# Kernel optimization log

Measured on AMD Instinct MI355X. Metric: run time of the kernel, lower is better.

## Reference

```python
import jax, jax.numpy as jnp
import numpy as np

NUM_EMBED = 1024
NUM_HEADS = 16
NUM_LAYER = 8
BLOCK_SIZE = 1024
VOCAB = 32000
B, T = 4, 1024
HEAD_SIZE = NUM_EMBED // NUM_HEADS


def _ln(x, g, b, eps=1e-5):
    mu = jnp.mean(x, axis=-1, keepdims=True)
    var = jnp.var(x, axis=-1, keepdims=True)
    return (x - mu) * jax.lax.rsqrt(var + eps) * g + b


def setup_inputs() -> dict:
    key = jax.random.key(0)
    ks = jax.random.split(key, 16)
    C, L, V = NUM_EMBED, NUM_LAYER, VOCAB
    std = 0.02
    n = lambda k, shp: jax.random.normal(k, shp, jnp.float32) * std
    return {
        "x": jax.random.randint(ks[0], (B, T), 0, V),
        "tok_emb": n(ks[1], (V, C)),
        "pos_emb": n(ks[2], (BLOCK_SIZE, C)),
        "Wq": n(ks[3], (L, C, C)),
        "Wk": n(ks[4], (L, C, C)),
        "Wv": n(ks[5], (L, C, C)),
        "Wproj": n(ks[6], (L, C, C)),
        "bproj": jnp.zeros((L, C), jnp.float32),
        "ln1_g": jnp.ones((L, C), jnp.float32),
        "ln1_b": jnp.zeros((L, C), jnp.float32),
        "ln2_g": jnp.ones((L, C), jnp.float32),
        "ln2_b": jnp.zeros((L, C), jnp.float32),
        "W1": n(ks[7], (L, C, 4 * C)),
        "b1": jnp.zeros((L, 4 * C), jnp.float32),
        "W2": n(ks[8], (L, 4 * C, C)),
        "b2": jnp.zeros((L, C), jnp.float32),
        "lnf_g": jnp.ones((C,), jnp.float32),
        "lnf_b": jnp.zeros((C,), jnp.float32),
        "Whead": n(ks[9], (C, V)),
    }


def _forward(x, tok_emb, pos_emb, Wq, Wk, Wv, Wproj, bproj,
             ln1_g, ln1_b, ln2_g, ln2_b, W1, b1, W2, b2,
             lnf_g, lnf_b, Whead):
    Bc, Tc = x.shape
    H, hs = NUM_HEADS, HEAD_SIZE
    h = tok_emb[x] + pos_emb[:Tc]  # [B,T,C]
    causal = jnp.tril(jnp.ones((Tc, Tc), bool))
    neg_inf = jnp.finfo(h.dtype).min
    for l in range(NUM_LAYER):
        xn = _ln(h, ln1_g[l], ln1_b[l])
        q = (xn @ Wq[l]).reshape(Bc, Tc, H, hs)
        k = (xn @ Wk[l]).reshape(Bc, Tc, H, hs)
        v = (xn @ Wv[l]).reshape(Bc, Tc, H, hs)
        att = jnp.einsum('bqhd,bkhd->bhqk', q, k) * (hs ** -0.5)
        att = jnp.where(causal, att, neg_inf)
        att = jax.nn.softmax(att, axis=-1)  # dropout p=0 in eval
        o = jnp.einsum('bhqk,bkhd->bqhd', att, v).reshape(Bc, Tc, H * hs)
        h = h + o @ Wproj[l] + bproj[l]
        xn = _ln(h, ln2_g[l], ln2_b[l])
        h = h + jax.nn.relu(xn @ W1[l] + b1[l]) @ W2[l] + b2[l]
    h = _ln(h, lnf_g, lnf_b)
    return h @ Whead  # logits [B,T,V]


def reference(x, tok_emb, pos_emb, Wq, Wk, Wv, Wproj, bproj,
              ln1_g, ln1_b, ln2_g, ln2_b, W1, b1, W2, b2,
              lnf_g, lnf_b, Whead):
    return _forward(x, tok_emb, pos_emb, Wq, Wk, Wv, Wproj, bproj,
                    ln1_g, ln1_b, ln2_g, ln2_b, W1, b1, W2, b2,
                    lnf_g, lnf_b, Whead)
```

## Files before the change

### kernel.cpp

```cpp
#include <hip/hip_runtime.h>
#include <stdint.h>
#include <stddef.h>

#define C_DIM 1024
#define T_DIM 1024
#define B_DIM 4
#define L_DIM 8
#define V_DIM 32000
#define HS 64
#define NHEAD 16
#define NROWS (B_DIM * T_DIM)
#define LDQ   3072
#define PROWS 65536

typedef __bf16 bf16_t;
typedef __attribute__((ext_vector_type(8))) __bf16 bf16x8;
typedef __attribute__((ext_vector_type(4))) __bf16 bf16x4;
typedef __attribute__((ext_vector_type(4))) float f32x4;
typedef unsigned int u32;
typedef unsigned short u16;

static __device__ __forceinline__ f32x4 mfma16(bf16x8 a, bf16x8 b, f32x4 c) {
    return __builtin_amdgcn_mfma_f32_16x16x32_bf16(a, b, c, 0, 0, 0);
}

static __device__ __forceinline__ void gl_lds16(const bf16_t* g, bf16_t* l) {
    __builtin_amdgcn_global_load_lds(
        (const __attribute__((address_space(1))) u32*)(const void*)g,
        (__attribute__((address_space(3))) u32*)(void*)l, 16, 0, 0);
}

__global__ __launch_bounds__(256) void embed_kernel(
    const int* __restrict__ x, const float* __restrict__ tok,
    const float* __restrict__ pos, float* __restrict__ h) {
    int idx = blockIdx.x * 256 + threadIdx.x;
    int row = idx >> 8;
    int c4  = (idx & 255) * 4;
    int t   = row & (T_DIM - 1);
    int tk  = x[row];
    float4 a = *(const float4*)(tok + (size_t)tk * C_DIM + c4);
    float4 p = *(const float4*)(pos + (size_t)t * C_DIM + c4);
    float4 r;
    r.x = a.x + p.x; r.y = a.y + p.y; r.z = a.z + p.z; r.w = a.w + p.w;
    *(float4*)(h + (size_t)row * C_DIM + c4) = r;
}

static __device__ __forceinline__ void wtr_tile(
    const float* __restrict__ in, bf16_t* __restrict__ out,
    int K, int N, int n0, int k0, int tid) {
    __shared__ float t[64][65];
    int tx = tid & 63, tw = tid >> 6;
#pragma unroll 4
    for (int i = 0; i < 16; ++i) {
        int k = tw * 16 + i;
        t[k][tx] = in[(size_t)(k0 + k) * N + n0 + tx];
    }
    __syncthreads();
#pragma unroll 4
    for (int i = 0; i < 16; ++i) {
        int n = tw * 16 + i;
        out[(size_t)(n0 + n) * K + k0 + tx] = (bf16_t)t[tx][n];
    }
}

__global__ __launch_bounds__(256) void wtr_kernel(
    const float* __restrict__ in, bf16_t* __restrict__ out, int K, int N) {
    wtr_tile(in, out, K, N, blockIdx.x * 64, blockIdx.y * 64, threadIdx.x);
}

__global__ __launch_bounds__(256) void ln_wtr_kernel(
    const float* __restrict__ x, const float* __restrict__ gam,
    const float* __restrict__ bet, bf16_t* __restrict__ out,
    const float* __restrict__ Wq, const float* __restrict__ Wk,
    const float* __restrict__ Wv, const float* __restrict__ Wp,
    const float* __restrict__ W1, const float* __restrict__ W2,
    bf16_t* __restrict__ qkvT, bf16_t* __restrict__ projT,
    bf16_t* __restrict__ w1T, bf16_t* __restrict__ w2T) {
    int bid = blockIdx.x;
    if (bid >= 1024) {
        int b = bid - 1024;
        const float* in; bf16_t* o2; int K, N, tn, tk;
        if (b < 1024) {
            int which = b >> 8, t = b & 255;
            in = which == 0 ? Wq : which == 1 ? Wk : which == 2 ? Wv : Wp;
            o2 = which < 3 ? qkvT + (size_t)which * C_DIM * C_DIM : projT;
            K = C_DIM; N = C_DIM; tn = t & 15; tk = t >> 4;
        } else if (b < 2048) {
            int t = b - 1024; in = W1; o2 = w1T;
            K = C_DIM; N = 4 * C_DIM; tn = t & 63; tk = t >> 6;
        } else {
            int t = b - 2048; in = W2; o2 = w2T;
            K = 4 * C_DIM; N = C_DIM; tn = t & 15; tk = t >> 4;
        }
        wtr_tile(in, o2, K, N, tn * 64, tk * 64, threadIdx.x);
        return;
    }
    int wave = threadIdx.x >> 6, lane = threadIdx.x & 63;
    int row  = bid * 4 + wave;
    const float* xr = x + (size_t)row * C_DIM;
    float4 v[4];
    float s = 0.f, sq = 0.f;
#pragma unroll
    for (int i = 0; i < 4; ++i) {
        v[i] = *(const float4*)(xr + i * 256 + lane * 4);
        s  += v[i].x + v[i].y + v[i].z + v[i].w;
        sq += v[i].x * v[i].x + v[i].y * v[i].y + v[i].z * v[i].z + v[i].w * v[i].w;
    }
#pragma unroll
    for (int m = 1; m < 64; m <<= 1) {
        s  += __shfl_xor(s, m);
        sq += __shfl_xor(sq, m);
    }
    float mu  = s * (1.f / 1024.f);
    float var = sq * (1.f / 1024.f) - mu * mu;
    float rs  = rsqrtf(var + 1e-5f);
    bf16_t* orow = out + (size_t)row * C_DIM;
#pragma unroll
    for (int i = 0; i < 4; ++i) {
        int c = i * 256 + lane * 4;
        float4 g4 = *(const float4*)(gam + c);
        float4 b4 = *(const float4*)(bet + c);
        bf16x4 o;
        o[0] = (bf16_t)((v[i].x - mu) * rs * g4.x + b4.x);
        o[1] = (bf16_t)((v[i].y - mu) * rs * g4.y + b4.y);
        o[2] = (bf16_t)((v[i].z - mu) * rs * g4.z + b4.z);
        o[3] = (bf16_t)((v[i].w - mu) * rs * g4.w + b4.w);
        *(bf16x4*)(orow + c) = o;
    }
}

__global__ __launch_bounds__(256) void ln_kernel(
    const float* __restrict__ x, const float* __restrict__ gam,
    const float* __restrict__ bet, bf16_t* __restrict__ out) {
    int wave = threadIdx.x >> 6, lane = threadIdx.x & 63;
    int row  = blockIdx.x * 4 + wave;
    const float* xr = x + (size_t)row * C_DIM;
    float4 v[4];
    float s = 0.f, sq = 0.f;
#pragma unroll
    for (int i = 0; i < 4; ++i) {
        v[i] = *(const float4*)(xr + i * 256 + lane * 4);
        s  += v[i].x + v[i].y + v[i].z + v[i].w;
        sq += v[i].x * v[i].x + v[i].y * v[i].y + v[i].z * v[i].z + v[i].w * v[i].w;
    }
#pragma unroll
    for (int m = 1; m < 64; m <<= 1) {
        s  += __shfl_xor(s, m);
        sq += __shfl_xor(sq, m);
    }
    float mu  = s * (1.f / 1024.f);
    float var = sq * (1.f / 1024.f) - mu * mu;
    float rs  = rsqrtf(var + 1e-5f);
    bf16_t* orow = out + (size_t)row * C_DIM;
#pragma unroll
    for (int i = 0; i < 4; ++i) {
        int c = i * 256 + lane * 4;
        float4 g4 = *(const float4*)(gam + c);
        float4 b4 = *(const float4*)(bet + c);
        bf16x4 o;
        o[0] = (bf16_t)((v[i].x - mu) * rs * g4.x + b4.x);
        o[1] = (bf16_t)((v[i].y - mu) * rs * g4.y + b4.y);
        o[2] = (bf16_t)((v[i].z - mu) * rs * g4.z + b4.z);
        o[3] = (bf16_t)((v[i].w - mu) * rs * g4.w + b4.w);
        *(bf16x4*)(orow + c) = o;
    }
}

template <int MODE>
__global__ __launch_bounds__(256) void gemm_kernel(
    const bf16_t* __restrict__ A, const bf16_t* __restrict__ Bt,
    const float* __restrict__ bias, void* __restrict__ Cout,
    int M, int N, int K, int KS) {
    __shared__ bf16_t Asm[2][128 * 32];
    __shared__ bf16_t Bsm[2][128 * 32];

    const int tid  = threadIdx.x;
    const int nwg  = gridDim.x;
    int bid = blockIdx.x;
    if ((nwg & 7) == 0) {
        int cpx = nwg >> 3;
        bid = (bid & 7) * cpx + (bid >> 3);
    }
    const int MT = M >> 7;
    const int nblk = MT * (N >> 7);
    const int kp = bid / nblk;
    bid %= nblk;
    const int mt = bid % MT, nt = bid / MT;
    const int mbase = mt << 7, nbase = nt << 7;
    const int wave = tid >> 6, lane = tid & 63;
    const int lr = lane & 15, lg = lane >> 4;
    const int wm = wave >> 1, wn = wave & 1;
    const int KL = K / KS;
    const int koff = kp * KL;
    const int NK = KL >> 5;

    const int srow = lane >> 2;
    const int ssw  = (((lane & 3) ^ ((lane >> 3) & 3)) << 3);
    const bf16_t* aRow = A  + (size_t)(mbase + wave * 32 + srow) * K + koff + ssw;
    const bf16_t* bRow = Bt + (size_t)(nbase + wave * 32 + srow) * K + koff + ssw;
    const int ldsW = wave * 1024;

#define STAGE(buf, kt)                                                        \
    do {                                                                      \
        const bf16_t* ag = aRow + (size_t)(kt) * 32;                          \
        const bf16_t* bg = bRow + (size_t)(kt) * 32;                          \
        gl_lds16(ag,            &Asm[buf][ldsW]);                             \
        gl_lds16(ag + 16 * K,   &Asm[buf][ldsW + 512]);                       \
        gl_lds16(bg,            &Bsm[buf][ldsW]);                             \
        gl_lds16(bg + 16 * K,   &Bsm[buf][ldsW + 512]);                       \
    } while (0)

    STAGE(0, 0);
    __syncthreads();

    f32x4 acc[4][4] = {};
    const int rsw = ((lg ^ ((lr >> 1) & 3)) << 3);
    int buf = 0;
    for (int kt = 0; kt < NK; ++kt) {
        if (kt + 1 < NK) STAGE(buf ^ 1, kt + 1);
        bf16x8 af[4], bfr[4];
#pragma unroll
        for (int i = 0; i < 4; ++i)
            af[i] = *(const bf16x8*)&Asm[buf][(wm * 64 + i * 16 + lr) * 32 + rsw];
#pragma unroll
        for (int j = 0; j < 4; ++j)
            bfr[j] = *(const bf16x8*)&Bsm[buf][(wn * 64 + j * 16 + lr) * 32 + rsw];
#pragma unroll
        for (int i = 0; i < 4; ++i)
#pragma unroll
            for (int j = 0; j < 4; ++j)
                acc[i][j] = mfma16(af[i], bfr[j], acc[i][j]);
        __syncthreads();
        buf ^= 1;
    }
#undef STAGE

    float bj[4];
#pragma unroll
    for (int j = 0; j < 4; ++j)
        bj[j] = (bias && kp == 0) ? bias[nbase + wn * 64 + j * 16 + lr] : 0.0f;
#pragma unroll
    for (int i = 0; i < 4; ++i) {
#pragma unroll
        for (int j = 0; j < 4; ++j) {
            int col = nbase + wn * 64 + j * 16 + lr;
#pragma unroll
            for (int e = 0; e < 4; ++e) {
                int row = mbase + wm * 64 + i * 16 + lg * 4 + e;
                float val = acc[i][j][e] + bj[j];
                size_t off = (size_t)row * N + col;
                if (MODE == 0) {
                    ((bf16_t*)Cout)[off] = (bf16_t)val;
                } else if (MODE == 1) {
                    ((bf16_t*)Cout)[off] = (bf16_t)fmaxf(val, 0.0f);
                } else {
                    atomicAdd(&((float*)Cout)[off], val);
                }
            }
        }
    }
}

template <int MODE>
__global__ __launch_bounds__(512, 4) void gemmW_kernel(
    const bf16_t* __restrict__ A, const bf16_t* __restrict__ Bt,
    const float* __restrict__ bias, void* __restrict__ Cout,
    int M, int N, int K) {
    __shared__ __align__(16) char smem[49152];
    bf16_t (*As)[128 * 32] = (bf16_t(*)[128 * 32])smem;
    bf16_t (*Bs)[256 * 32] = (bf16_t(*)[256 * 32])(smem + 16384);

    const int tid  = threadIdx.x;
    const int nwg  = gridDim.x;
    int bid = blockIdx.x;
    if ((nwg & 7) == 0) {
        int cpx = nwg >> 3;
        bid = (bid & 7) * cpx + (bid >> 3);
    }
    const int MT = M >> 7;
    const int mt = bid % MT, nt = bid / MT;
    const int mbase = mt << 7, nbase = nt << 8;
    const int wave = tid >> 6, lane = tid & 63;
    const int lr = lane & 15, lg = lane >> 4;
    const int wm64 = (wave >> 2) * 64;
    const int wn64 = (wave & 3) * 64;
    const int NK = K >> 5;

    const int srow = tid >> 2;
    const int csrc = (((tid & 3) ^ ((tid >> 3) & 3)) << 3);
    const bf16_t* aPtr = A  + (size_t)(mbase + srow) * K + csrc;
    const bf16_t* b0   = Bt + (size_t)(nbase + srow) * K + csrc;
    const bf16_t* b1   = b0 + (size_t)128 * K;
    const int ldsW = wave * 512;

#define STAGEW(buf, kt)                                                       \
    do {                                                                      \
        gl_lds16(aPtr + (size_t)(kt) * 32, &As[buf][ldsW]);                   \
        gl_lds16(b0   + (size_t)(kt) * 32, &Bs[buf][ldsW]);                   \
        gl_lds16(b1   + (size_t)(kt) * 32, &Bs[buf][4096 + ldsW]);            \
    } while (0)

    STAGEW(0, 0);
    __syncthreads();

    f32x4 acc[4][4] = {};
    const int rofs = ((lg ^ ((lr >> 1) & 3)) << 3);
    int buf = 0;
    for (int kt = 0; kt < NK; ++kt) {
        if (kt + 1 < NK) STAGEW(buf ^ 1, kt + 1);
        bf16x8 af[4], bfr[4];
#pragma unroll
        for (int i = 0; i < 4; ++i)
            af[i] = *(const bf16x8*)&As[buf][(wm64 + i * 16 + lr) * 32 + rofs];
#pragma unroll
        for (int j = 0; j < 4; ++j)
            bfr[j] = *(const bf16x8*)&Bs[buf][(wn64 + j * 16 + lr) * 32 + rofs];
#pragma unroll
        for (int i = 0; i < 4; ++i)
#pragma unroll
            for (int j = 0; j < 4; ++j)
                acc[i][j] = mfma16(af[i], bfr[j], acc[i][j]);
        __syncthreads();
        buf ^= 1;
    }
#undef STAGEW

    float bj[4];
#pragma unroll
    for (int j = 0; j < 4; ++j)
        bj[j] = bias ? bias[nbase + wn64 + j * 16 + lr] : 0.0f;

    if (MODE == 3) {
        float* tw = (float*)smem + wave * (16 * 68);
#pragma unroll
        for (int i = 0; i < 4; ++i) {
#pragma unroll
            for (int j = 0; j < 4; ++j)
#pragma unroll
                for (int e = 0; e < 4; ++e)
                    tw[(lg * 4 + e) * 68 + j * 16 + lr] = acc[i][j][e] + bj[j];
            asm volatile("s_waitcnt lgkmcnt(0)" ::: "memory");
#pragma unroll
            for (int ss = 0; ss < 4; ++ss) {
                int rr = ss * 4 + lg;
                f32x4 v = *(const f32x4*)&tw[rr * 68 + lr * 4];
                size_t off = (size_t)(mbase + wm64 + i * 16 + rr) * N
                           + (nbase + wn64 + lr * 4);
                __builtin_nontemporal_store(v, (f32x4*)&((float*)Cout)[off]);
            }
            asm volatile("s_waitcnt lgkmcnt(0)" ::: "memory");
        }
        return;
    }

#pragma unroll
    for (int i = 0; i < 4; ++i) {
#pragma unroll
        for (int j = 0; j < 4; ++j) {
            int col = nbase + wn64 + j * 16 + lr;
#pragma unroll
            for (int e = 0; e < 4; ++e) {
                int row = mbase + wm64 + i * 16 + lg * 4 + e;
                float val = acc[i][j][e] + bj[j];
                size_t off = (size_t)row * N + col;
                if (MODE == 0) {
                    ((bf16_t*)Cout)[off] = (bf16_t)val;
                } else {
                    ((bf16_t*)Cout)[off] = (bf16_t)fmaxf(val, 0.0f);
                }
            }
        }
    }
}

__global__ __launch_bounds__(256) void attn_kernel(
    const bf16_t* __restrict__ Qb, const bf16_t* __restrict__ Kb,
    const bf16_t* __restrict__ Vb, float* __restrict__ Opart,
    float* __restrict__ Lbuf) {
    __shared__ bf16_t Ksm[2][64][72];
    __shared__ bf16_t Vsm[2][64][72];
    __shared__ bf16_t Psm[4][32][72];

    const int tid  = threadIdx.x;
    const int bid  = blockIdx.x;
    const int rank = bid >> 6;
    const int qt   = 7 - (rank >> 1);
    const int half = rank & 1;
    const int bh   = bid & 63;
    const int hh   = bh & 15;
    const int bb   = bh >> 4;
    const int t0   = half ? (qt + 1) : 0;
    const int t1   = half ? (2 * qt + 2) : (qt + 1);
    const int wave = tid >> 6, lane = tid & 63;
    const int lr = lane & 15, lg = lane >> 4;
    const int qbase = qt * 128 + wave * 32;
    const size_t basei = ((size_t)bb * T_DIM) * LDQ + hh * HS;
    const int pg = bh * 8 + qt;

    bf16x8 qf[2][2];
#pragma unroll
    for (int rb = 0; rb < 2; ++rb) {
        const bf16_t* qrow = Qb + basei + (size_t)(qbase + rb * 16 + lr) * LDQ;
        qf[rb][0] = *(const bf16x8*)(qrow + lg * 8);
        qf[rb][1] = *(const bf16x8*)(qrow + 32 + lg * 8);
    }

    f32x4 o[2][4] = {};
    float psum[2][4];
#pragma unroll
    for (int rb = 0; rb < 2; ++rb)
#pragma unroll
        for (int e = 0; e < 4; ++e) psum[rb][e] = 0.f;

    const int krow = tid >> 2, kc = (tid & 3) * 8;
    const bf16_t* kgp = Kb + basei + (size_t)krow * LDQ + kc;
    const int vds = (tid & 7) * 8, vkg = (tid >> 3) * 2;
    const bf16_t* vgp0 = Vb + basei + (size_t)vkg * LDQ + vds;
    const bf16_t* vgp1 = vgp0 + LDQ;

    uint4 k0r, k1r, v0r, v1r;
    {
        const size_t g0 = (size_t)t0 * 64 * LDQ;
        k0r = *(const uint4*)(kgp + g0);
        k1r = *(const uint4*)(kgp + g0 + 32);
        v0r = *(const uint4*)(vgp0 + g0);
        v1r = *(const uint4*)(vgp1 + g0);
    }
    *(uint4*)&Ksm[0][krow][kc]      = k0r;
    *(uint4*)&Ksm[0][krow][kc + 32] = k1r;
    {
        const u16* e0 = (const u16*)&v0r;
        const u16* e1 = (const u16*)&v1r;
#pragma unroll
        for (int j = 0; j < 8; ++j)
            *(u32*)&Vsm[0][vds + j][vkg] = (u32)e0[j] | ((u32)e1[j] << 16);
    }
    __syncthreads();

    const float SCL = 0.18033688011112042f;
    for (int kt = t0; kt < t1; ++kt) {
        const int c = (kt - t0) & 1;
        if (kt + 1 < t1) {
            const size_t go = (size_t)(kt + 1) * 64 * LDQ;
            k0r = *(const uint4*)(kgp + go);
            k1r = *(const uint4*)(kgp + go + 32);
            v0r = *(const uint4*)(vgp0 + go);
            v1r = *(const uint4*)(vgp1 + go);
        }

        f32x4 s[2][4];
        __builtin_amdgcn_s_setprio(1);
#pragma unroll
        for (int kk = 0; kk < 4; ++kk) {
            bf16x8 kf0 = *(const bf16x8*)&Ksm[c][kk * 16 + lr][lg * 8];
            bf16x8 kf1 = *(const bf16x8*)&Ksm[c][kk * 16 + lr][32 + lg * 8];
#pragma unroll
            for (int rb = 0; rb < 2; ++rb) {
                f32x4 z = {};
                z = mfma16(qf[rb][0], kf0, z);
                z = mfma16(qf[rb][1], kf1, z);
                s[rb][kk] = z;
            }
        }
        __builtin_amdgcn_s_setprio(0);
        if (kt * 64 + 63 > qbase) {
#pragma unroll
            for (int rb = 0; rb < 2; ++rb)
#pragma unroll
                for (int kk = 0; kk < 4; ++kk)
#pragma unroll
                    for (int e = 0; e < 4; ++e) {
                        int key = kt * 64 + kk * 16 + lr;
                        int qi  = qbase + rb * 16 + lg * 4 + e;
                        float v = s[rb][kk][e] * SCL;
                        s[rb][kk][e] = (key <= qi) ? v : -1e30f;
                    }
        } else {
#pragma unroll
            for (int rb = 0; rb < 2; ++rb)
#pragma unroll
                for (int kk = 0; kk < 4; ++kk)
#pragma unroll
                    for (int e = 0; e < 4; ++e)
                        s[rb][kk][e] *= SCL;
        }

#pragma unroll
        for (int rb = 0; rb < 2; ++rb) {
#pragma unroll
            for (int e = 0; e < 4; ++e) {
                float p0 = exp2f(s[rb][0][e]);
                float p1 = exp2f(s[rb][1][e]);
                float p2 = exp2f(s[rb][2][e]);
                float p3 = exp2f(s[rb][3][e]);
                int qrow = rb * 16 + lg * 4 + e;
                Psm[wave][qrow][lr]      = (bf16_t)p0;
                Psm[wave][qrow][16 + lr] = (bf16_t)p1;
                Psm[wave][qrow][32 + lr] = (bf16_t)p2;
                Psm[wave][qrow][48 + lr] = (bf16_t)p3;
                psum[rb][e] += (p0 + p1) + (p2 + p3);
            }
        }

        asm volatile("s_waitcnt lgkmcnt(0)" ::: "memory");
        bf16x8 pf[2][2];
#pragma unroll
        for (int rb = 0; rb < 2; ++rb)
#pragma unroll
            for (int h2 = 0; h2 < 2; ++h2)
                pf[rb][h2] = *(const bf16x8*)&Psm[wave][rb * 16 + lr][h2 * 32 + lg * 8];
        __builtin_amdgcn_s_setprio(1);
#pragma unroll
        for (int h2 = 0; h2 < 2; ++h2)
#pragma unroll
            for (int db = 0; db < 4; ++db) {
                bf16x8 vf = *(const bf16x8*)&Vsm[c][db * 16 + lr][h2 * 32 + lg * 8];
#pragma unroll
                for (int rb = 0; rb < 2; ++rb)
                    o[rb][db] = mfma16(pf[rb][h2], vf, o[rb][db]);
            }
        __builtin_amdgcn_s_setprio(0);

        if (kt + 1 < t1) {
            const int w = c ^ 1;
            *(uint4*)&Ksm[w][krow][kc]      = k0r;
            *(uint4*)&Ksm[w][krow][kc + 32] = k1r;
            const u16* e0 = (const u16*)&v0r;
            const u16* e1 = (const u16*)&v1r;
#pragma unroll
            for (int j = 0; j < 8; ++j)
                *(u32*)&Vsm[w][vds + j][vkg] = (u32)e0[j] | ((u32)e1[j] << 16);
        }
        __syncthreads();
    }

    const size_t prow0 = (size_t)half * PROWS + (size_t)pg * 128 + wave * 32;
#pragma unroll
    for (int rb = 0; rb < 2; ++rb)
#pragma unroll
        for (int e = 0; e < 4; ++e) {
            float l = psum[rb][e];
            l += __shfl_xor(l, 1);
            l += __shfl_xor(l, 2);
            l += __shfl_xor(l, 4);
            l += __shfl_xor(l, 8);
            size_t row = prow0 + rb * 16 + lg * 4 + e;
            float* op = Opart + row * 64;
#pragma unroll
            for (int db = 0; db < 4; ++db)
                op[db * 16 + lr] = o[rb][db][e];
            if (lr == 0) Lbuf[row] = l;
        }
}

__global__ __launch_bounds__(256) void attn_merge_kernel(
    const float* __restrict__ Opart, const float* __restrict__ Lbuf,
    bf16_t* __restrict__ Ob) {
    int idx = blockIdx.x * 256 + threadIdx.x;
    int row = idx >> 4, d4 = (idx & 15) * 4;
    float l0 = Lbuf[row];
    float l1 = Lbuf[(size_t)PROWS + row];
    float inv = 1.0f / (l0 + l1);
    float4 a = *(const float4*)&Opart[(size_t)row * 64 + d4];
    float4 b = *(const float4*)&Opart[((size_t)PROWS + row) * 64 + d4];
    bf16x4 r;
    r[0] = (bf16_t)((a.x + b.x) * inv);
    r[1] = (bf16_t)((a.y + b.y) * inv);
    r[2] = (bf16_t)((a.z + b.z) * inv);
    r[3] = (bf16_t)((a.w + b.w) * inv);
    int pg = row >> 7, rloc = row & 127;
    int bh = pg >> 3, qt = pg & 7;
    int bb = bh >> 4, hh = bh & 15;
    *(bf16x4*)&Ob[((size_t)bb * T_DIM + qt * 128 + rloc) * C_DIM + hh * HS + d4] = r;
}

extern "C" void kernel_launch(void* const* d_in, const int* in_sizes, int n_in,
                              void* d_out, int out_size, void* d_ws, size_t ws_size,
                              hipStream_t stream) {
    const int*   x      = (const int*)d_in[0];
    const float* tok    = (const float*)d_in[1];
    const float* pos    = (const float*)d_in[2];
    const float* Wq     = (const float*)d_in[3];
    const float* Wk     = (const float*)d_in[4];
    const float* Wv     = (const float*)d_in[5];
    const float* Wproj  = (const float*)d_in[6];
    const float* bproj  = (const float*)d_in[7];
    const float* ln1_g  = (const float*)d_in[8];
    const float* ln1_b  = (const float*)d_in[9];
    const float* ln2_g  = (const float*)d_in[10];
    const float* ln2_b  = (const float*)d_in[11];
    const float* W1     = (const float*)d_in[12];
    const float* b1     = (const float*)d_in[13];
    const float* W2     = (const float*)d_in[14];
    const float* b2     = (const float*)d_in[15];
    const float* lnf_g  = (const float*)d_in[16];
    const float* lnf_b  = (const float*)d_in[17];
    const float* Whead  = (const float*)d_in[18];
    float* out = (float*)d_out;

    char* ws = (char*)d_ws;
    float*  h    = (float*)ws;   ws += (size_t)NROWS * C_DIM * 4;
    bf16_t* xn   = (bf16_t*)ws;  ws += (size_t)NROWS * C_DIM * 2;
    bf16_t* qkvb = (bf16_t*)ws;  ws += (size_t)NROWS * LDQ * 2;
    bf16_t* ob   = (bf16_t*)ws;  ws += (size_t)NROWS * C_DIM * 2;
    bf16_t* mid  = (bf16_t*)ws;  ws += (size_t)NROWS * 4 * C_DIM * 2;
    bf16_t* wT   = (bf16_t*)ws;  ws += (size_t)V_DIM * C_DIM * 2;
    float*  opart = (float*)ws;  ws += (size_t)2 * PROWS * 64 * 4;
    float*  lbuf  = (float*)ws;  ws += (size_t)2 * PROWS * 4;

    const size_t M1 = (size_t)C_DIM * C_DIM;
    bf16_t* qkvT  = wT;
    bf16_t* projT = wT + 3 * M1;
    bf16_t* w1T   = wT + 4 * M1;
    bf16_t* w2T   = wT + 8 * M1;

    dim3 blk(256);
    dim3 blk512(512);

    embed_kernel<<<dim3(NROWS * C_DIM / 1024), blk, 0, stream>>>(x, tok, pos, h);

    for (int l = 0; l < L_DIM; ++l) {
        const size_t wo  = (size_t)l * M1;
        const size_t wo1 = (size_t)l * 4 * M1;

        ln_wtr_kernel<<<dim3(1024 + 3072), blk, 0, stream>>>(
            h, ln1_g + l * C_DIM, ln1_b + l * C_DIM, xn,
            Wq + wo, Wk + wo, Wv + wo, Wproj + wo, W1 + wo1, W2 + wo1,
            qkvT, projT, w1T, w2T);

        gemmW_kernel<0><<<dim3(32 * 12), blk512, 0, stream>>>(
            xn, qkvT, nullptr, qkvb, NROWS, LDQ, C_DIM);

        attn_kernel<<<dim3(1024), blk, 0, stream>>>(
            qkvb, qkvb + C_DIM, qkvb + 2 * C_DIM, opart, lbuf);
        attn_merge_kernel<<<dim3(PROWS * 16 / 256), blk, 0, stream>>>(
            opart, lbuf, ob);

        gemm_kernel<2><<<dim3(32 * 8 * 2), blk, 0, stream>>>(
            ob, projT, bproj + l * C_DIM, h, NROWS, C_DIM, C_DIM, 2);

        ln_kernel<<<dim3(NROWS / 4), blk, 0, stream>>>(h, ln2_g + l * C_DIM, ln2_b + l * C_DIM, xn);

        gemmW_kernel<1><<<dim3(32 * 16), blk512, 0, stream>>>(
            xn, w1T, b1 + (size_t)l * 4 * C_DIM, mid, NROWS, 4 * C_DIM, C_DIM);

        gemm_kernel<2><<<dim3(32 * 8 * 2), blk, 0, stream>>>(
            mid, w2T, b2 + l * C_DIM, h, NROWS, C_DIM, 4 * C_DIM, 2);
    }

    ln_kernel<<<dim3(NROWS / 4), blk, 0, stream>>>(h, lnf_g, lnf_b, xn);
    wtr_kernel<<<dim3(500, 16), blk, 0, stream>>>(Whead, wT, C_DIM, V_DIM);
    gemmW_kernel<3><<<dim3(32 * 125), blk512, 0, stream>>>(
        xn, wT, nullptr, out, NROWS, V_DIM, C_DIM);
}
```

Before: 2.301 ms.

## Drop split-K attention and merge kernel; each block handles full key range

```diff
diff --git a/kernel.cpp b/kernel.cpp
--- a/kernel.cpp
+++ b/kernel.cpp
@@ -11,7 +11,6 @@
 #define NHEAD 16
 #define NROWS (B_DIM * T_DIM)
 #define LDQ   3072
-#define PROWS 65536
 
 typedef __bf16 bf16_t;
 typedef __attribute__((ext_vector_type(8))) __bf16 bf16x8;
@@ -375,27 +374,23 @@
 
 __global__ __launch_bounds__(256) void attn_kernel(
     const bf16_t* __restrict__ Qb, const bf16_t* __restrict__ Kb,
-    const bf16_t* __restrict__ Vb, float* __restrict__ Opart,
-    float* __restrict__ Lbuf) {
+    const bf16_t* __restrict__ Vb, bf16_t* __restrict__ Ob) {
     __shared__ bf16_t Ksm[2][64][72];
     __shared__ bf16_t Vsm[2][64][72];
     __shared__ bf16_t Psm[4][32][72];
 
     const int tid  = threadIdx.x;
     const int bid  = blockIdx.x;
-    const int rank = bid >> 6;
-    const int qt   = 7 - (rank >> 1);
-    const int half = rank & 1;
+    const int qt   = 7 - (bid >> 6);
     const int bh   = bid & 63;
     const int hh   = bh & 15;
     const int bb   = bh >> 4;
-    const int t0   = half ? (qt + 1) : 0;
-    const int t1   = half ? (2 * qt + 2) : (qt + 1);
+    const int nkt  = 2 * qt + 2;
     const int wave = tid >> 6, lane = tid & 63;
     const int lr = lane & 15, lg = lane >> 4;
     const int qbase = qt * 128 + wave * 32;
     const size_t basei = ((size_t)bb * T_DIM) * LDQ + hh * HS;
-    const int pg = bh * 8 + qt;
+    const size_t baseo = ((size_t)bb * T_DIM) * C_DIM + hh * HS;
 
     bf16x8 qf[2][2];
 #pragma unroll
@@ -419,13 +414,10 @@
     const bf16_t* vgp1 = vgp0 + LDQ;
 
     uint4 k0r, k1r, v0r, v1r;
-    {
-        const size_t g0 = (size_t)t0 * 64 * LDQ;
-        k0r = *(const uint4*)(kgp + g0);
-        k1r = *(const uint4*)(kgp + g0 + 32);
-        v0r = *(const uint4*)(vgp0 + g0);
-        v1r = *(const uint4*)(vgp1 + g0);
-    }
+    k0r = *(const uint4*)(kgp);
+    k1r = *(const uint4*)(kgp + 32);
+    v0r = *(const uint4*)(vgp0);
+    v1r = *(const uint4*)(vgp1);
     *(uint4*)&Ksm[0][krow][kc]      = k0r;
     *(uint4*)&Ksm[0][krow][kc + 32] = k1r;
     {
@@ -438,9 +430,9 @@
     __syncthreads();
 
     const float SCL = 0.18033688011112042f;
-    for (int kt = t0; kt < t1; ++kt) {
-        const int c = (kt - t0) & 1;
-        if (kt + 1 < t1) {
+    for (int kt = 0; kt < nkt; ++kt) {
+        const int c = kt & 1;
+        if (kt + 1 < nkt) {
             const size_t go = (size_t)(kt + 1) * 64 * LDQ;
             k0r = *(const uint4*)(kgp + go);
             k1r = *(const uint4*)(kgp + go + 32);
@@ -521,7 +513,7 @@
             }
         __builtin_amdgcn_s_setprio(0);
 
-        if (kt + 1 < t1) {
+        if (kt + 1 < nkt) {
             const int w = c ^ 1;
             *(uint4*)&Ksm[w][krow][kc]      = k0r;
             *(uint4*)&Ksm[w][krow][kc + 32] = k1r;
@@ -534,7 +526,6 @@
         __syncthreads();
     }
 
-    const size_t prow0 = (size_t)half * PROWS + (size_t)pg * 128 + wave * 32;
 #pragma unroll
     for (int rb = 0; rb < 2; ++rb)
 #pragma unroll
@@ -544,34 +535,12 @@
             l += __shfl_xor(l, 2);
             l += __shfl_xor(l, 4);
             l += __shfl_xor(l, 8);
-            size_t row = prow0 + rb * 16 + lg * 4 + e;
-            float* op = Opart + row * 64;
+            float inv = 1.0f / l;
+            bf16_t* orow = Ob + baseo + (size_t)(qbase + rb * 16 + lg * 4 + e) * C_DIM;
 #pragma unroll
             for (int db = 0; db < 4; ++db)
-                op[db * 16 + lr] = o[rb][db][e];
-            if (lr == 0) Lbuf[row] = l;
-        }
-}
-
-__global__ __launch_bounds__(256) void attn_merge_kernel(
-    const float* __restrict__ Opart, const float* __restrict__ Lbuf,
-    bf16_t* __restrict__ Ob) {
-    int idx = blockIdx.x * 256 + threadIdx.x;
-    int row = idx >> 4, d4 = (idx & 15) * 4;
-    float l0 = Lbuf[row];
-    float l1 = Lbuf[(size_t)PROWS + row];
-    float inv = 1.0f / (l0 + l1);
-    float4 a = *(const float4*)&Opart[(size_t)row * 64 + d4];
-    float4 b = *(const float4*)&Opart[((size_t)PROWS + row) * 64 + d4];
-    bf16x4 r;
-    r[0] = (bf16_t)((a.x + b.x) * inv);
-    r[1] = (bf16_t)((a.y + b.y) * inv);
-    r[2] = (bf16_t)((a.z + b.z) * inv);
-    r[3] = (bf16_t)((a.w + b.w) * inv);
-    int pg = row >> 7, rloc = row & 127;
-    int bh = pg >> 3, qt = pg & 7;
-    int bb = bh >> 4, hh = bh & 15;
-    *(bf16x4*)&Ob[((size_t)bb * T_DIM + qt * 128 + rloc) * C_DIM + hh * HS + d4] = r;
+                orow[db * 16 + lr] = (bf16_t)(o[rb][db][e] * inv);
+        }
 }
 
 extern "C" void kernel_launch(void* const* d_in, const int* in_sizes, int n_in,
@@ -605,8 +574,6 @@
     bf16_t* ob   = (bf16_t*)ws;  ws += (size_t)NROWS * C_DIM * 2;
     bf16_t* mid  = (bf16_t*)ws;  ws += (size_t)NROWS * 4 * C_DIM * 2;
     bf16_t* wT   = (bf16_t*)ws;  ws += (size_t)V_DIM * C_DIM * 2;
-    float*  opart = (float*)ws;  ws += (size_t)2 * PROWS * 64 * 4;
-    float*  lbuf  = (float*)ws;  ws += (size_t)2 * PROWS * 4;
 
     const size_t M1 = (size_t)C_DIM * C_DIM;
     bf16_t* qkvT  = wT;
@@ -631,10 +598,8 @@
         gemmW_kernel<0><<<dim3(32 * 12), blk512, 0, stream>>>(
             xn, qkvT, nullptr, qkvb, NROWS, LDQ, C_DIM);
 
-        attn_kernel<<<dim3(1024), blk, 0, stream>>>(
-            qkvb, qkvb + C_DIM, qkvb + 2 * C_DIM, opart, lbuf);
-        attn_merge_kernel<<<dim3(PROWS * 16 / 256), blk, 0, stream>>>(
-            opart, lbuf, ob);
+        attn_kernel<<<dim3(512), blk, 0, stream>>>(
+            qkvb, qkvb + C_DIM, qkvb + 2 * C_DIM, ob);
 
         gemm_kernel<2><<<dim3(32 * 8 * 2), blk, 0, stream>>>(
             ob, projT, bproj + l * C_DIM, h, NROWS, C_DIM, C_DIM, 2);
```

Measured after the change: 2.274 ms (median of 2 runs). Within noise of the previous version (-1.1%).
